# Optimization experiments

Measured on AMD Instinct MI355X. Metric: run time of the kernel, lower is better.

The kernel has to match this reference:

```python
import jax, jax.numpy as jnp
import numpy as np


def setup_inputs() -> dict:
    key = jax.random.key(0)
    k0, k1, k2 = jax.random.split(key, 3)
    B, C, N, M = 2, 64, 1024, 32
    C_mid = 16  # bottleneck of the AFA weight-learning MLP (C -> C//4 -> C)
    feature = jax.random.normal(k0, (B, C, N, M), dtype=jnp.float32)
    W1 = (jax.random.normal(k1, (C_mid, C), dtype=jnp.float32) / np.float32(np.sqrt(C)))
    b1 = jnp.zeros((C_mid,), dtype=jnp.float32)
    W2 = (jax.random.normal(k2, (C, C_mid), dtype=jnp.float32) / np.float32(np.sqrt(C_mid)))
    b2 = jnp.zeros((C,), dtype=jnp.float32)
    return {"feature": feature, "W1": W1, "b1": b1, "W2": W2, "b2": b2}


def reference(feature, W1, b1, W2, b2):
    # feature: (B, C, N, M)
    B, C, N, M = feature.shape
    eye = jnp.eye(M, dtype=feature.dtype)  # (M, M)
    # pair[b,c,n,i,j] = f_i - f_j + f_i * delta_ij  (the repeat/transpose/eye trick)
    fi = feature[..., :, None]                      # (B, C, N, M, 1)
    pair = fi - feature[..., None, :] + fi * eye    # (B, C, N, M, M)
    # 1x1-conv MLP over channel dim (SharedMLP: C -> C_mid -> C), ReLU between
    h = jax.nn.relu(jnp.einsum('oc,bcnij->bonij', W1, pair)
                    + b1[None, :, None, None, None])
    w = (jnp.einsum('oc,bcnij->bonij', W2, h)
         + b2[None, :, None, None, None])           # (B, C, N, M, M)
    w = jax.nn.softmax(w, axis=-1)                  # use_softmax=True, over last dim
    # weighted-sum aggregation over j -> (B, C, N, M)
    return jnp.sum(pair * w, axis=-1)
```

## Files before the change

### kernel.cpp

```cpp
#include <hip/hip_runtime.h>
#include <stdint.h>

namespace {
constexpr int NM = 1024 * 32;
constexpr float LOG2E = 1.44269504088896340736f;

typedef _Float16 half8 __attribute__((ext_vector_type(8)));
typedef float floatx16 __attribute__((ext_vector_type(16)));
typedef float f2v __attribute__((ext_vector_type(2)));

__device__ __forceinline__ uint32_t pkrtz_bits(float a, float b) {
  auto pk = __builtin_amdgcn_cvt_pkrtz(a, b);
  uint32_t u;
  __builtin_memcpy(&u, &pk, 4);
  return u;
}

__global__ __launch_bounds__(256, 4) void afa_kernel(
    const float* __restrict__ feat,
    const float* __restrict__ W1,
    const float* __restrict__ b1,
    const float* __restrict__ W2,
    float* __restrict__ out)
{
  __shared__ __align__(16) float f_c[64 * 34];
  __shared__ __align__(16) float g1b[32 * 20];
  __shared__ __align__(16) float w1s[16 * 68];
  __shared__ __align__(16) float edia[64 * 34];
  __shared__ __align__(16) float outs[64 * 34];

  const int t = threadIdx.x;
  const int bn = blockIdx.x;
  const size_t base = (size_t)(bn >> 10) * (64 * NM) + (size_t)(bn & 1023) * 32;

  const int w  = t >> 6;
  const int ln = t & 63;
  const int cl = ln & 31;
  const int hl = ln >> 5;

  half8 B0, B1;
  {
    const float4* w2a = reinterpret_cast<const float4*>(W2 + cl * 16 + 8 * hl);
    const float4 x = w2a[0], y = w2a[1];
    B0[0] = (_Float16)(x.x * LOG2E); B0[1] = (_Float16)(x.y * LOG2E);
    B0[2] = (_Float16)(x.z * LOG2E); B0[3] = (_Float16)(x.w * LOG2E);
    B0[4] = (_Float16)(y.x * LOG2E); B0[5] = (_Float16)(y.y * LOG2E);
    B0[6] = (_Float16)(y.z * LOG2E); B0[7] = (_Float16)(y.w * LOG2E);
    const float4* w2b = reinterpret_cast<const float4*>(W2 + (cl + 32) * 16 + 8 * hl);
    const float4 u = w2b[0], v = w2b[1];
    B1[0] = (_Float16)(u.x * LOG2E); B1[1] = (_Float16)(u.y * LOG2E);
    B1[2] = (_Float16)(u.z * LOG2E); B1[3] = (_Float16)(u.w * LOG2E);
    B1[4] = (_Float16)(v.x * LOG2E); B1[5] = (_Float16)(v.y * LOG2E);
    B1[6] = (_Float16)(v.z * LOG2E); B1[7] = (_Float16)(v.w * LOG2E);
  }
  const float b1a = b1[t >> 5];
  const float b1b = b1[(t >> 5) + 8];

  {
    const int o = t >> 4, cq = t & 15;
    reinterpret_cast<float4*>(w1s)[o * 17 + cq] =
        reinterpret_cast<const float4*>(W1)[t];
  }
  {
    const int m = t & 31, c0 = t >> 5;
    #pragma unroll
    for (int r = 0; r < 8; ++r) {
      const int c = c0 + 8 * r;
      f_c[c * 34 + m] = feat[base + (size_t)c * NM + m];
    }
  }
  __syncthreads();

  {
    const int m = t & 31, o2 = t >> 5;
    const float* wa = w1s + o2 * 68;
    const float* wb = w1s + (o2 + 8) * 68;
    float a0 = b1a, a1 = b1b;
    #pragma unroll
    for (int c = 0; c < 64; ++c) {
      const float v = f_c[c * 34 + m];
      a0 = fmaf(wa[c], v, a0);
      a1 = fmaf(wb[c], v, a1);
    }
    g1b[m * 20 + o2] = a0;
    g1b[m * 20 + o2 + 8] = a1;
  }

  float fcol0[16], fcol1[16];
  #pragma unroll
  for (int q = 0; q < 4; ++q) {
    const int jr = 8 * q + 4 * hl;
    const float2 a0 = *reinterpret_cast<const float2*>(f_c + cl * 34 + jr);
    const float2 a1 = *reinterpret_cast<const float2*>(f_c + cl * 34 + jr + 2);
    fcol0[4 * q]     = a0.x; fcol0[4 * q + 1] = a0.y;
    fcol0[4 * q + 2] = a1.x; fcol0[4 * q + 3] = a1.y;
    const float2 c0v = *reinterpret_cast<const float2*>(f_c + (cl + 32) * 34 + jr);
    const float2 c1v = *reinterpret_cast<const float2*>(f_c + (cl + 32) * 34 + jr + 2);
    fcol1[4 * q]     = c0v.x; fcol1[4 * q + 1] = c0v.y;
    fcol1[4 * q + 2] = c1v.x; fcol1[4 * q + 3] = c1v.y;
  }
  __syncthreads();

  floatx16 Z;
  #pragma unroll
  for (int r = 0; r < 16; ++r) Z[r] = 0.f;

  float gjn[8];
  {
    const float4* gp = reinterpret_cast<const float4*>(g1b + cl * 20 + 8 * hl);
    const float4 x = gp[0], y = gp[1];
    const float gj[8] = {x.x, x.y, x.z, x.w, y.x, y.y, y.z, y.w};
    const float4* bb = reinterpret_cast<const float4*>(b1 + 8 * hl);
    const float4 bx = bb[0], by = bb[1];
    const float b1r[8] = {bx.x, bx.y, bx.z, bx.w, by.x, by.y, by.z, by.w};
    #pragma unroll
    for (int q = 0; q < 8; ++q) gjn[q] = b1r[q] - gj[q];

    if (w == 0) {
      union { half8 h; uint32_t u[4]; } au;
      #pragma unroll
      for (int p = 0; p < 4; ++p) {
        au.u[p] = pkrtz_bits(fmaxf(gj[2 * p], 0.f), fmaxf(gj[2 * p + 1], 0.f));
      }
      floatx16 d0 = __builtin_amdgcn_mfma_f32_32x32x16_f16(au.h, B0, Z, 0, 0, 0);
      floatx16 d1 = __builtin_amdgcn_mfma_f32_32x32x16_f16(au.h, B1, Z, 0, 0, 0);
      #pragma unroll
      for (int r = 0; r < 16; ++r) {
        const int ir = (r & 3) + 8 * (r >> 2) + 4 * hl;
        edia[cl * 34 + ir]        = __builtin_amdgcn_exp2f(d0[r]);
        edia[(cl + 32) * 34 + ir] = __builtin_amdgcn_exp2f(d1[r]);
      }
    }
  }
  __syncthreads();

  #pragma unroll 1
  for (int ii = 0; ii < 8; ++ii) {
    const int i = w * 8 + ii;
    const bool dg = (cl == i);
    const float4* gi4 = reinterpret_cast<const float4*>(g1b + i * 20 + 8 * hl);
    const float4 gx = gi4[0], gy = gi4[1];
    const float gi[8] = {gx.x, gx.y, gx.z, gx.w, gy.x, gy.y, gy.z, gy.w};
    union { half8 h; uint32_t u[4]; } au;
    #pragma unroll
    for (int p = 0; p < 4; ++p) {
      const float h0 = fmaxf(gi[2 * p]     + (dg ? 0.f : gjn[2 * p]),     0.f);
      const float h1 = fmaxf(gi[2 * p + 1] + (dg ? 0.f : gjn[2 * p + 1]), 0.f);
      au.u[p] = pkrtz_bits(h0, h1);
    }
    const floatx16 acc0 = __builtin_amdgcn_mfma_f32_32x32x16_f16(au.h, B0, Z, 0, 0, 0);
    const floatx16 acc1 = __builtin_amdgcn_mfma_f32_32x32x16_f16(au.h, B1, Z, 0, 0, 0);

    f2v S0 = {0.f, 0.f}, D0 = {0.f, 0.f}, S1 = {0.f, 0.f}, D1 = {0.f, 0.f};
    #pragma unroll
    for (int r = 0; r < 16; r += 2) {
      const f2v e0 = {__builtin_amdgcn_exp2f(acc0[r]),
                      __builtin_amdgcn_exp2f(acc0[r + 1])};
      const f2v fc0 = {fcol0[r], fcol0[r + 1]};
      S0 += e0;
      D0 += fc0 * e0;
      const f2v e1 = {__builtin_amdgcn_exp2f(acc1[r]),
                      __builtin_amdgcn_exp2f(acc1[r + 1])};
      const f2v fc1 = {fcol1[r], fcol1[r + 1]};
      S1 += e1;
      D1 += fc1 * e1;
    }
    float Sa = S0.x + S0.y, Da = D0.x + D0.y;
    float Sb = S1.x + S1.y, Db = D1.x + D1.y;
    Sa += __shfl_xor(Sa, 32); Da += __shfl_xor(Da, 32);
    Sb += __shfl_xor(Sb, 32); Db += __shfl_xor(Db, 32);

    const float fi0 = f_c[cl * 34 + i];
    const float fi1 = f_c[(cl + 32) * 34 + i];
    const float ei0 = edia[cl * 34 + i];
    const float ei1 = edia[(cl + 32) * 34 + i];
    const float inv0 = 1.0f / Sa;
    const float inv1 = 1.0f / Sb;
    outs[cl * 34 + i]        = fi0 * (1.0f + ei0 * inv0) - Da * inv0;
    outs[(cl + 32) * 34 + i] = fi1 * (1.0f + ei1 * inv1) - Db * inv1;
  }
  __syncthreads();

  {
    const int m = t & 31, c0 = t >> 5;
    #pragma unroll
    for (int r = 0; r < 8; ++r) {
      const int cc = c0 + 8 * r;
      out[base + (size_t)cc * NM + m] = outs[cc * 34 + m];
    }
  }
}
}

extern "C" void kernel_launch(void* const* d_in, const int* in_sizes, int n_in,
                              void* d_out, int out_size, void* d_ws, size_t ws_size,
                              hipStream_t stream) {
  const float* feat = (const float*)d_in[0];
  const float* W1   = (const float*)d_in[1];
  const float* b1   = (const float*)d_in[2];
  const float* W2   = (const float*)d_in[3];
  float* out = (float*)d_out;

  afa_kernel<<<dim3(2 * 1024), dim3(256), 0, stream>>>(feat, W1, b1, W2, out);
}
```

Before: 31.97 us.

## Split channel tiles across waves and alias W1/diag-exp LDS to raise occupancy

Each wave now handles a single 32-channel tile (tile = w&1) over 16 rows i, instead of both channel tiles over 8 rows. This halves per-thread B fragments, fcol arrays and accumulators, so launch bounds go from 4 to 6 blocks per CU. The diagonal exp values are stored as fp16 in a buffer that aliases the W1 staging area, which cuts LDS per block. The costs are reduced precision on the diagonal term and a longer serial loop per wave.

Result: slower. 34.55 us (+8.1%).

```diff
diff --git a/kernel.cpp b/kernel.cpp
--- a/kernel.cpp
+++ b/kernel.cpp
@@ -16,7 +16,7 @@
   return u;
 }
 
-__global__ __launch_bounds__(256, 4) void afa_kernel(
+__global__ __launch_bounds__(256, 6) void afa_kernel(
     const float* __restrict__ feat,
     const float* __restrict__ W1,
     const float* __restrict__ b1,
@@ -25,33 +25,32 @@
 {
   __shared__ __align__(16) float f_c[64 * 34];
   __shared__ __align__(16) float g1b[32 * 20];
-  __shared__ __align__(16) float w1s[16 * 68];
-  __shared__ __align__(16) float edia[64 * 34];
+  __shared__ __align__(16) float u1[16 * 68];
   __shared__ __align__(16) float outs[64 * 34];
+
+  float* const w1s = u1;
+  _Float16* const edia = reinterpret_cast<_Float16*>(u1);
 
   const int t = threadIdx.x;
   const int bn = blockIdx.x;
   const size_t base = (size_t)(bn >> 10) * (64 * NM) + (size_t)(bn & 1023) * 32;
 
-  const int w  = t >> 6;
-  const int ln = t & 63;
-  const int cl = ln & 31;
-  const int hl = ln >> 5;
+  const int w    = t >> 6;
+  const int ln   = t & 63;
+  const int cl   = ln & 31;
+  const int hl   = ln >> 5;
+  const int tile = w & 1;
+  const int ih   = w >> 1;
+  const int ct   = cl + 32 * tile;
 
-  half8 B0, B1;
+  half8 B;
   {
-    const float4* w2a = reinterpret_cast<const float4*>(W2 + cl * 16 + 8 * hl);
-    const float4 x = w2a[0], y = w2a[1];
-    B0[0] = (_Float16)(x.x * LOG2E); B0[1] = (_Float16)(x.y * LOG2E);
-    B0[2] = (_Float16)(x.z * LOG2E); B0[3] = (_Float16)(x.w * LOG2E);
-    B0[4] = (_Float16)(y.x * LOG2E); B0[5] = (_Float16)(y.y * LOG2E);
-    B0[6] = (_Float16)(y.z * LOG2E); B0[7] = (_Float16)(y.w * LOG2E);
-    const float4* w2b = reinterpret_cast<const float4*>(W2 + (cl + 32) * 16 + 8 * hl);
-    const float4 u = w2b[0], v = w2b[1];
-    B1[0] = (_Float16)(u.x * LOG2E); B1[1] = (_Float16)(u.y * LOG2E);
-    B1[2] = (_Float16)(u.z * LOG2E); B1[3] = (_Float16)(u.w * LOG2E);
-    B1[4] = (_Float16)(v.x * LOG2E); B1[5] = (_Float16)(v.y * LOG2E);
-    B1[6] = (_Float16)(v.z * LOG2E); B1[7] = (_Float16)(v.w * LOG2E);
+    const float4* w2p = reinterpret_cast<const float4*>(W2 + ct * 16 + 8 * hl);
+    const float4 x = w2p[0], y = w2p[1];
+    B[0] = (_Float16)(x.x * LOG2E); B[1] = (_Float16)(x.y * LOG2E);
+    B[2] = (_Float16)(x.z * LOG2E); B[3] = (_Float16)(x.w * LOG2E);
+    B[4] = (_Float16)(y.x * LOG2E); B[5] = (_Float16)(y.y * LOG2E);
+    B[6] = (_Float16)(y.z * LOG2E); B[7] = (_Float16)(y.w * LOG2E);
   }
   const float b1a = b1[t >> 5];
   const float b1b = b1[(t >> 5) + 8];
@@ -86,18 +85,14 @@
     g1b[m * 20 + o2 + 8] = a1;
   }
 
-  float fcol0[16], fcol1[16];
+  float fcol[16];
   #pragma unroll
   for (int q = 0; q < 4; ++q) {
     const int jr = 8 * q + 4 * hl;
-    const float2 a0 = *reinterpret_cast<const float2*>(f_c + cl * 34 + jr);
-    const float2 a1 = *reinterpret_cast<const float2*>(f_c + cl * 34 + jr + 2);
-    fcol0[4 * q]     = a0.x; fcol0[4 * q + 1] = a0.y;
-    fcol0[4 * q + 2] = a1.x; fcol0[4 * q + 3] = a1.y;
-    const float2 c0v = *reinterpret_cast<const float2*>(f_c + (cl + 32) * 34 + jr);
-    const float2 c1v = *reinterpret_cast<const float2*>(f_c + (cl + 32) * 34 + jr + 2);
-    fcol1[4 * q]     = c0v.x; fcol1[4 * q + 1] = c0v.y;
-    fcol1[4 * q + 2] = c1v.x; fcol1[4 * q + 3] = c1v.y;
+    const float2 a0 = *reinterpret_cast<const float2*>(f_c + ct * 34 + jr);
+    const float2 a1 = *reinterpret_cast<const float2*>(f_c + ct * 34 + jr + 2);
+    fcol[4 * q]     = a0.x; fcol[4 * q + 1] = a0.y;
+    fcol[4 * q + 2] = a1.x; fcol[4 * q + 3] = a1.y;
   }
   __syncthreads();
 
@@ -116,27 +111,25 @@
     #pragma unroll
     for (int q = 0; q < 8; ++q) gjn[q] = b1r[q] - gj[q];
 
-    if (w == 0) {
+    if (w < 2) {
       union { half8 h; uint32_t u[4]; } au;
       #pragma unroll
       for (int p = 0; p < 4; ++p) {
         au.u[p] = pkrtz_bits(fmaxf(gj[2 * p], 0.f), fmaxf(gj[2 * p + 1], 0.f));
       }
-      floatx16 d0 = __builtin_amdgcn_mfma_f32_32x32x16_f16(au.h, B0, Z, 0, 0, 0);
-      floatx16 d1 = __builtin_amdgcn_mfma_f32_32x32x16_f16(au.h, B1, Z, 0, 0, 0);
+      const floatx16 d = __builtin_amdgcn_mfma_f32_32x32x16_f16(au.h, B, Z, 0, 0, 0);
       #pragma unroll
       for (int r = 0; r < 16; ++r) {
         const int ir = (r & 3) + 8 * (r >> 2) + 4 * hl;
-        edia[cl * 34 + ir]        = __builtin_amdgcn_exp2f(d0[r]);
-        edia[(cl + 32) * 34 + ir] = __builtin_amdgcn_exp2f(d1[r]);
+        edia[ct * 34 + ir] = (_Float16)__builtin_amdgcn_exp2f(d[r]);
       }
     }
   }
   __syncthreads();
 
   #pragma unroll 1
-  for (int ii = 0; ii < 8; ++ii) {
-    const int i = w * 8 + ii;
+  for (int ii = 0; ii < 16; ++ii) {
+    const int i = 16 * ih + ii;
     const bool dg = (cl == i);
     const float4* gi4 = reinterpret_cast<const float4*>(g1b + i * 20 + 8 * hl);
     const float4 gx = gi4[0], gy = gi4[1];
@@ -148,36 +141,25 @@
       const float h1 = fmaxf(gi[2 * p + 1] + (dg ? 0.f : gjn[2 * p + 1]), 0.f);
       au.u[p] = pkrtz_bits(h0, h1);
     }
-    const floatx16 acc0 = __builtin_amdgcn_mfma_f32_32x32x16_f16(au.h, B0, Z, 0, 0, 0);
-    const floatx16 acc1 = __builtin_amdgcn_mfma_f32_32x32x16_f16(au.h, B1, Z, 0, 0, 0);
+    const floatx16 acc = __builtin_amdgcn_mfma_f32_32x32x16_f16(au.h, B, Z, 0, 0, 0);
 
-    f2v S0 = {0.f, 0.f}, D0 = {0.f, 0.f}, S1 = {0.f, 0.f}, D1 = {0.f, 0.f};
+    f2v S = {0.f, 0.f}, D = {0.f, 0.f};
     #pragma unroll
     for (int r = 0; r < 16; r += 2) {
-      const f2v e0 = {__builtin_amdgcn_exp2f(acc0[r]),
-                      __builtin_amdgcn_exp2f(acc0[r + 1])};
-      const f2v fc0 = {fcol0[r], fcol0[r + 1]};
-      S0 += e0;
-      D0 += fc0 * e0;
-      const f2v e1 = {__builtin_amdgcn_exp2f(acc1[r]),
-                      __builtin_amdgcn_exp2f(acc1[r + 1])};
-      const f2v fc1 = {fcol1[r], fcol1[r + 1]};
-      S1 += e1;
-      D1 += fc1 * e1;
+      const f2v e = {__builtin_amdgcn_exp2f(acc[r]),
+                     __builtin_amdgcn_exp2f(acc[r + 1])};
+      const f2v fc = {fcol[r], fcol[r + 1]};
+      S += e;
+      D += fc * e;
     }
-    float Sa = S0.x + S0.y, Da = D0.x + D0.y;
-    float Sb = S1.x + S1.y, Db = D1.x + D1.y;
-    Sa += __shfl_xor(Sa, 32); Da += __shfl_xor(Da, 32);
-    Sb += __shfl_xor(Sb, 32); Db += __shfl_xor(Db, 32);
+    float Sa = S.x + S.y, Da = D.x + D.y;
+    Sa += __shfl_xor(Sa, 32);
+    Da += __shfl_xor(Da, 32);
 
-    const float fi0 = f_c[cl * 34 + i];
-    const float fi1 = f_c[(cl + 32) * 34 + i];
-    const float ei0 = edia[cl * 34 + i];
-    const float ei1 = edia[(cl + 32) * 34 + i];
-    const float inv0 = 1.0f / Sa;
-    const float inv1 = 1.0f / Sb;
-    outs[cl * 34 + i]        = fi0 * (1.0f + ei0 * inv0) - Da * inv0;
-    outs[(cl + 32) * 34 + i] = fi1 * (1.0f + ei1 * inv1) - Db * inv1;
+    const float fi = f_c[ct * 34 + i];
+    const float ei = (float)edia[ct * 34 + i];
+    const float inv = 1.0f / Sa;
+    outs[ct * 34 + i] = fi * (1.0f + ei * inv) - Da * inv;
   }
   __syncthreads();
 
```
